# Optimization experiments

Hardware: AMD Instinct MI355X
Metric: run time of the kernel (lower is better)

The kernel has to match this reference:

```python
import jax, jax.numpy as jnp
import numpy as np

EMBED_SIZE = 768
HEAD_SIZE = 64
B, T = 4, 2048


def setup_inputs() -> dict:
    key = jax.random.key(0)
    kx, kk, kq, kv = jax.random.split(key, 4)
    x = jax.random.normal(kx, (B, T, EMBED_SIZE), dtype=jnp.float32)
    # torch Linear(E, H, bias=False): weight [H, E]; stored here as [E, H] for x @ W
    s = 1.0 / np.sqrt(EMBED_SIZE)
    Wk = jax.random.uniform(kk, (EMBED_SIZE, HEAD_SIZE), jnp.float32, -s, s)
    Wq = jax.random.uniform(kq, (EMBED_SIZE, HEAD_SIZE), jnp.float32, -s, s)
    Wv = jax.random.uniform(kv, (EMBED_SIZE, HEAD_SIZE), jnp.float32, -s, s)
    return {"x": x, "Wk": Wk, "Wq": Wq, "Wv": Wv}


def reference(x, Wk, Wq, Wv):
    Bx, Tx, E = x.shape
    k = x @ Wk  # [B, T, H]
    q = x @ Wq
    v = x @ Wv
    w = jnp.einsum("bth,bsh->bts", q, k)  # [B, T, T]
    causal = jnp.tril(jnp.ones((Tx, Tx), dtype=bool))
    # Faithful to source: mask to -inf FIRST, then scale by sqrt(embed_size)
    w = jnp.where(causal, w, -jnp.inf)
    w = w / jnp.sqrt(jnp.asarray(E, dtype=x.dtype))
    w = jax.nn.softmax(w, axis=-1)
    # dropout: eval mode / identity for the correctness baseline
    return jnp.einsum("bts,bsh->bth", w, v)
```

## Files before the change

kernel.cpp:

```cpp
#include <hip/hip_runtime.h>
#include <hip/hip_bf16.h>


typedef __attribute__((ext_vector_type(8))) short short8;
typedef __attribute__((ext_vector_type(4))) float f32x4;

#define SPLIT_KB 4
#define MAX_SP 8

__device__ __forceinline__ unsigned short f2bf(float f) {
    union { float f; unsigned u; } v; v.f = f;
    unsigned r = v.u + 0x7fffu + ((v.u >> 16) & 1u);
    return (unsigned short)(r >> 16);
}

__global__ __launch_bounds__(256) void proj_kernel(const float* __restrict__ x,
                                                   const float* __restrict__ Wk,
                                                   const float* __restrict__ Wq,
                                                   const float* __restrict__ Wv,
                                                   unsigned short* __restrict__ qws,
                                                   unsigned short* __restrict__ kws,
                                                   unsigned short* __restrict__ vT) {
    __shared__ unsigned short xs[32 * 72];
    __shared__ unsigned short wsm[64 * 72];
    const float CSCALE = 1.4426950408889634f / 27.712812921102035f;
    int tid = threadIdx.x;
    int lane = tid & 63, wave = tid >> 6;
    int quad = lane >> 4, l16 = lane & 15;
    int row0 = blockIdx.x * 32;
    int my = blockIdx.y;
    const float* W = (my == 0) ? Wq : (my == 1) ? Wk : Wv;

    int xrow = tid >> 3, xcb = (tid & 7) * 8;
    int wn = tid & 63, wk0 = (tid >> 6) * 16;

    f32x4 acc[2];
    acc[0] = (f32x4)(0.f); acc[1] = (f32x4)(0.f);

    for (int kc = 0; kc < 12; ++kc) {
        __syncthreads();
        {
            const float* src = x + (size_t)(row0 + xrow) * 768 + kc * 64 + xcb;
            float4 f0 = *(const float4*)(src);
            float4 f1 = *(const float4*)(src + 4);
            short8 pk;
            pk[0] = (short)f2bf(f0.x); pk[1] = (short)f2bf(f0.y);
            pk[2] = (short)f2bf(f0.z); pk[3] = (short)f2bf(f0.w);
            pk[4] = (short)f2bf(f1.x); pk[5] = (short)f2bf(f1.y);
            pk[6] = (short)f2bf(f1.z); pk[7] = (short)f2bf(f1.w);
            *(short8*)&xs[xrow * 72 + xcb] = pk;
        }
        {
            float wv[16];
            for (int i = 0; i < 16; ++i)
                wv[i] = W[(size_t)(kc * 64 + wk0 + i) * 64 + wn];
            if (my == 0)
                for (int i = 0; i < 16; ++i) wv[i] *= CSCALE;
            short8 p0, p1;
            for (int i = 0; i < 8; ++i) { p0[i] = (short)f2bf(wv[i]); p1[i] = (short)f2bf(wv[8 + i]); }
            *(short8*)&wsm[wn * 72 + wk0] = p0;
            *(short8*)&wsm[wn * 72 + wk0 + 8] = p1;
        }
        __syncthreads();
        for (int kh = 0; kh < 2; ++kh) {
            int kk = kh * 32 + quad * 8;
            short8 bfr = *(const short8*)&wsm[(wave * 16 + l16) * 72 + kk];
            for (int mt = 0; mt < 2; ++mt) {
                short8 a = *(const short8*)&xs[(mt * 16 + l16) * 72 + kk];
                acc[mt] = __builtin_amdgcn_mfma_f32_16x16x32_bf16(a, bfr, acc[mt], 0, 0, 0);
            }
        }
    }
    __syncthreads();
    int n = wave * 16 + l16;
    if (my != 2) {
        unsigned short* dst = (my == 0) ? qws : kws;
        for (int mt = 0; mt < 2; ++mt)
            for (int j = 0; j < 4; ++j) {
                int rloc = mt * 16 + quad * 4 + j;
                dst[(size_t)(row0 + rloc) * 64 + n] = f2bf(acc[mt][j]);
            }
    } else {
        for (int mt = 0; mt < 2; ++mt)
            for (int j = 0; j < 4; ++j) {
                int rloc = mt * 16 + quad * 4 + j;
                wsm[n * 40 + rloc] = f2bf(acc[mt][j]);
            }
        __syncthreads();
        int bidx = row0 >> 11, t0 = row0 & 2047;
        int c = tid >> 2, rb = (tid & 3) * 8;
        *(short8*)&vT[((size_t)(bidx * 64 + c)) * 2048 + t0 + rb] =
            *(const short8*)&wsm[c * 40 + rb];
    }
}

__global__ __launch_bounds__(128) void attn_split(const unsigned short* __restrict__ qws,
                                                  const unsigned short* __restrict__ kws,
                                                  const unsigned short* __restrict__ vT,
                                                  float* __restrict__ po,
                                                  float* __restrict__ pm,
                                                  float* __restrict__ pl,
                                                  float* __restrict__ out) {
    int bx = blockIdx.x, b = blockIdx.y, sp = blockIdx.z;
    int kbmax = (bx >> 1) + 1;
    int nsp = (kbmax + SPLIT_KB - 1) / SPLIT_KB;
    if (sp >= nsp) return;
    int kb_lo = sp * SPLIT_KB;
    int kb_hi = min(kb_lo + SPLIT_KB, kbmax);

    __shared__ unsigned short qs[32 * 72];
    __shared__ unsigned short ks[64 * 72];
    __shared__ unsigned short vs[64 * 72];
    __shared__ unsigned short ps[2][16 * 72];
    int tid = threadIdx.x;
    int lane = tid & 63, wave = tid >> 6;
    int quad = lane >> 4, l16 = lane & 15;
    int q0 = bx * 32;
    size_t qbase = ((size_t)b * 2048 + q0) * 64;
    for (int i = 0; i < 2; ++i) {
        int e = tid + 128 * i;
        int r = e >> 3, hb = (e & 7) * 8;
        *(short8*)&qs[r * 72 + hb] = *(const short8*)&qws[qbase + r * 64 + hb];
    }
    __syncthreads();
    short8 aq[2];
    for (int kh = 0; kh < 2; ++kh)
        aq[kh] = *(const short8*)&qs[(wave * 16 + l16) * 72 + kh * 32 + quad * 8];

    f32x4 o_acc[4];
    for (int nt = 0; nt < 4; ++nt) o_acc[nt] = (f32x4)(0.f);
    float m_run[4], l_run[4];
    int row_g[4];
    for (int j = 0; j < 4; ++j) {
        m_run[j] = -1e30f; l_run[j] = 0.f;
        row_g[j] = q0 + wave * 16 + quad * 4 + j;
    }

    for (int kb = kb_lo; kb < kb_hi; ++kb) {
        __syncthreads();
        size_t kvbase = ((size_t)b * 2048 + kb * 64) * 64;
        for (int i = 0; i < 4; ++i) {
            int e = tid + 128 * i;
            int r = e >> 3, hb = (e & 7) * 8;
            *(short8*)&ks[r * 72 + hb] = *(const short8*)&kws[kvbase + r * 64 + hb];
        }
        for (int i = 0; i < 4; ++i) {
            int e = tid + 128 * i;
            int h = e >> 3, kyb = (e & 7) * 8;
            *(short8*)&vs[h * 72 + kyb] =
                *(const short8*)&vT[((size_t)b * 64 + h) * 2048 + kb * 64 + kyb];
        }
        __syncthreads();
        f32x4 s[4];
        for (int nt = 0; nt < 4; ++nt) s[nt] = (f32x4)(0.f);
        for (int kh = 0; kh < 2; ++kh)
            for (int nt = 0; nt < 4; ++nt) {
                short8 bk = *(const short8*)&ks[(nt * 16 + l16) * 72 + kh * 32 + quad * 8];
                s[nt] = __builtin_amdgcn_mfma_f32_16x16x32_bf16(aq[kh], bk, s[nt], 0, 0, 0);
            }
        if (kb == kbmax - 1) {
            for (int nt = 0; nt < 4; ++nt) {
                int key = kb * 64 + nt * 16 + l16;
                for (int j = 0; j < 4; ++j)
                    if (key > row_g[j]) s[nt][j] = -1e30f;
            }
        }
        float mx[4], al[4], rs[4];
        for (int j = 0; j < 4; ++j)
            mx[j] = fmaxf(fmaxf(s[0][j], s[1][j]), fmaxf(s[2][j], s[3][j]));
        for (int off = 1; off < 16; off <<= 1)
            for (int j = 0; j < 4; ++j)
                mx[j] = fmaxf(mx[j], __shfl_xor(mx[j], off, 16));
        for (int j = 0; j < 4; ++j) {
            float mn = fmaxf(m_run[j], mx[j]);
            al[j] = exp2f(m_run[j] - mn);
            m_run[j] = mn;
            rs[j] = 0.f;
        }
        for (int nt = 0; nt < 4; ++nt)
            for (int j = 0; j < 4; ++j) {
                float p = exp2f(s[nt][j] - m_run[j]);
                rs[j] += p;
                ps[wave][(quad * 4 + j) * 72 + nt * 16 + l16] = f2bf(p);
            }
        for (int off = 1; off < 16; off <<= 1)
            for (int j = 0; j < 4; ++j)
                rs[j] += __shfl_xor(rs[j], off, 16);
        for (int j = 0; j < 4; ++j) l_run[j] = l_run[j] * al[j] + rs[j];
        for (int nt = 0; nt < 4; ++nt)
            for (int j = 0; j < 4; ++j) o_acc[nt][j] *= al[j];
        for (int kh = 0; kh < 2; ++kh) {
            short8 ap = *(const short8*)&ps[wave][l16 * 72 + kh * 32 + quad * 8];
            for (int nt = 0; nt < 4; ++nt) {
                short8 bv = *(const short8*)&vs[(nt * 16 + l16) * 72 + kh * 32 + quad * 8];
                o_acc[nt] = __builtin_amdgcn_mfma_f32_16x16x32_bf16(ap, bv, o_acc[nt], 0, 0, 0);
            }
        }
    }
    if (nsp == 1) {
        for (int nt = 0; nt < 4; ++nt)
            for (int j = 0; j < 4; ++j)
                out[((size_t)b * 2048 + row_g[j]) * 64 + nt * 16 + l16] =
                    o_acc[nt][j] / l_run[j];
        return;
    }
    int sbase = ((b * 64 + bx) * MAX_SP + sp) * 32;
    for (int nt = 0; nt < 4; ++nt)
        for (int j = 0; j < 4; ++j) {
            int r = wave * 16 + quad * 4 + j;
            po[(size_t)(sbase + r) * 64 + nt * 16 + l16] = o_acc[nt][j];
        }
    if (l16 == 0) {
        for (int j = 0; j < 4; ++j) {
            int r = wave * 16 + quad * 4 + j;
            pm[sbase + r] = m_run[j];
            pl[sbase + r] = l_run[j];
        }
    }
}

__global__ __launch_bounds__(256) void reduce_kernel(const float* __restrict__ po,
                                                     const float* __restrict__ pm,
                                                     const float* __restrict__ pl,
                                                     float* __restrict__ out) {
    int tid = threadIdx.x;
    int lane = tid & 63, wave = tid >> 6;
    int g = blockIdx.x * 4 + wave;
    int b = g >> 11, t = g & 2047;
    int bx = t >> 5, r = t & 31;
    int kbmax = (bx >> 1) + 1;
    int nsp = (kbmax + SPLIT_KB - 1) / SPLIT_KB;
    if (nsp == 1) return;
    int base = ((b * 64 + bx) * MAX_SP) * 32 + r;
    float mstar = -1e30f;
    for (int sp = 0; sp < nsp; ++sp)
        mstar = fmaxf(mstar, pm[base + sp * 32]);
    float acc = 0.f, lsum = 0.f;
    for (int sp = 0; sp < nsp; ++sp) {
        float w = exp2f(pm[base + sp * 32] - mstar);
        acc += w * po[(size_t)(base + sp * 32) * 64 + lane];
        lsum += w * pl[base + sp * 32];
    }
    out[(size_t)g * 64 + lane] = acc / lsum;
}

extern "C" void kernel_launch(void* const* d_in, const int* in_sizes, int n_in,
                              void* d_out, int out_size, void* d_ws, size_t ws_size,
                              hipStream_t stream) {
    const float* x  = (const float*)d_in[0];
    const float* Wk = (const float*)d_in[1];
    const float* Wq = (const float*)d_in[2];
    const float* Wv = (const float*)d_in[3];
    float* out = (float*)d_out;
    char* w = (char*)d_ws;
    unsigned short* qws = (unsigned short*)w;
    unsigned short* kws = (unsigned short*)(w + 1048576);
    unsigned short* vT  = (unsigned short*)(w + 2097152);
    float* po = (float*)(w + 3145728);
    float* pm = (float*)(w + 19922944);
    float* pl = (float*)(w + 20185088);
    proj_kernel<<<dim3(256, 3), 256, 0, stream>>>(x, Wk, Wq, Wv, qws, kws, vT);
    attn_split<<<dim3(64, 4, MAX_SP), 128, 0, stream>>>(qws, kws, vT, po, pm, pl, out);
    reduce_kernel<<<2048, 256, 0, stream>>>(po, pm, pl, out);
}
```

Baseline: 109.8 us.

## Use single-wave attention blocks loading K/V fragments directly from global memory

The attention kernel changes from 128-thread blocks covering 32 query rows to 64-thread single-wave blocks covering 16 rows, with twice as many blocks. Q, K and V MFMA operands are read straight from global memory into registers, so the shared-memory staging and the block barriers go away. Only a small per-wave P buffer stays in LDS. The price is that K/V reuse across waves is lost, so each wave fetches its own K/V tiles (L2 traffic roughly doubles), and the global loads are strided short8 reads.

```diff
diff --git a/kernel.cpp b/kernel.cpp
--- a/kernel.cpp
+++ b/kernel.cpp
@@ -94,38 +94,28 @@
     }
 }
 
-__global__ __launch_bounds__(128) void attn_split(const unsigned short* __restrict__ qws,
-                                                  const unsigned short* __restrict__ kws,
-                                                  const unsigned short* __restrict__ vT,
-                                                  float* __restrict__ po,
-                                                  float* __restrict__ pm,
-                                                  float* __restrict__ pl,
-                                                  float* __restrict__ out) {
+__global__ __launch_bounds__(64) void attn_split(const unsigned short* __restrict__ qws,
+                                                 const unsigned short* __restrict__ kws,
+                                                 const unsigned short* __restrict__ vT,
+                                                 float* __restrict__ po,
+                                                 float* __restrict__ pm,
+                                                 float* __restrict__ pl,
+                                                 float* __restrict__ out) {
     int bx = blockIdx.x, b = blockIdx.y, sp = blockIdx.z;
-    int kbmax = (bx >> 1) + 1;
+    int kbmax = (bx >> 2) + 1;
     int nsp = (kbmax + SPLIT_KB - 1) / SPLIT_KB;
     if (sp >= nsp) return;
     int kb_lo = sp * SPLIT_KB;
     int kb_hi = min(kb_lo + SPLIT_KB, kbmax);
 
-    __shared__ unsigned short qs[32 * 72];
-    __shared__ unsigned short ks[64 * 72];
-    __shared__ unsigned short vs[64 * 72];
-    __shared__ unsigned short ps[2][16 * 72];
-    int tid = threadIdx.x;
-    int lane = tid & 63, wave = tid >> 6;
+    __shared__ unsigned short ps[16 * 72];
+    int lane = threadIdx.x & 63;
     int quad = lane >> 4, l16 = lane & 15;
-    int q0 = bx * 32;
-    size_t qbase = ((size_t)b * 2048 + q0) * 64;
-    for (int i = 0; i < 2; ++i) {
-        int e = tid + 128 * i;
-        int r = e >> 3, hb = (e & 7) * 8;
-        *(short8*)&qs[r * 72 + hb] = *(const short8*)&qws[qbase + r * 64 + hb];
-    }
-    __syncthreads();
-    short8 aq[2];
-    for (int kh = 0; kh < 2; ++kh)
-        aq[kh] = *(const short8*)&qs[(wave * 16 + l16) * 72 + kh * 32 + quad * 8];
+    int q0 = bx * 16;
+
+    const unsigned short* qp = qws + ((size_t)b * 2048 + q0 + l16) * 64 + quad * 8;
+    short8 aq0 = *(const short8*)(qp);
+    short8 aq1 = *(const short8*)(qp + 32);
 
     f32x4 o_acc[4];
     for (int nt = 0; nt < 4; ++nt) o_acc[nt] = (f32x4)(0.f);
@@ -133,31 +123,20 @@
     int row_g[4];
     for (int j = 0; j < 4; ++j) {
         m_run[j] = -1e30f; l_run[j] = 0.f;
-        row_g[j] = q0 + wave * 16 + quad * 4 + j;
+        row_g[j] = q0 + quad * 4 + j;
     }
 
     for (int kb = kb_lo; kb < kb_hi; ++kb) {
-        __syncthreads();
-        size_t kvbase = ((size_t)b * 2048 + kb * 64) * 64;
-        for (int i = 0; i < 4; ++i) {
-            int e = tid + 128 * i;
-            int r = e >> 3, hb = (e & 7) * 8;
-            *(short8*)&ks[r * 72 + hb] = *(const short8*)&kws[kvbase + r * 64 + hb];
-        }
-        for (int i = 0; i < 4; ++i) {
-            int e = tid + 128 * i;
-            int h = e >> 3, kyb = (e & 7) * 8;
-            *(short8*)&vs[h * 72 + kyb] =
-                *(const short8*)&vT[((size_t)b * 64 + h) * 2048 + kb * 64 + kyb];
-        }
-        __syncthreads();
+        const unsigned short* kp =
+            kws + ((size_t)b * 2048 + kb * 64 + l16) * 64 + quad * 8;
         f32x4 s[4];
         for (int nt = 0; nt < 4; ++nt) s[nt] = (f32x4)(0.f);
-        for (int kh = 0; kh < 2; ++kh)
-            for (int nt = 0; nt < 4; ++nt) {
-                short8 bk = *(const short8*)&ks[(nt * 16 + l16) * 72 + kh * 32 + quad * 8];
-                s[nt] = __builtin_amdgcn_mfma_f32_16x16x32_bf16(aq[kh], bk, s[nt], 0, 0, 0);
-            }
+        for (int nt = 0; nt < 4; ++nt) {
+            short8 bk0 = *(const short8*)(kp + (size_t)nt * 16 * 64);
+            short8 bk1 = *(const short8*)(kp + (size_t)nt * 16 * 64 + 32);
+            s[nt] = __builtin_amdgcn_mfma_f32_16x16x32_bf16(aq0, bk0, s[nt], 0, 0, 0);
+            s[nt] = __builtin_amdgcn_mfma_f32_16x16x32_bf16(aq1, bk1, s[nt], 0, 0, 0);
+        }
         if (kb == kbmax - 1) {
             for (int nt = 0; nt < 4; ++nt) {
                 int key = kb * 64 + nt * 16 + l16;
@@ -181,7 +160,7 @@
             for (int j = 0; j < 4; ++j) {
                 float p = exp2f(s[nt][j] - m_run[j]);
                 rs[j] += p;
-                ps[wave][(quad * 4 + j) * 72 + nt * 16 + l16] = f2bf(p);
+                ps[(quad * 4 + j) * 72 + nt * 16 + l16] = f2bf(p);
             }
         for (int off = 1; off < 16; off <<= 1)
             for (int j = 0; j < 4; ++j)
@@ -189,10 +168,12 @@
         for (int j = 0; j < 4; ++j) l_run[j] = l_run[j] * al[j] + rs[j];
         for (int nt = 0; nt < 4; ++nt)
             for (int j = 0; j < 4; ++j) o_acc[nt][j] *= al[j];
+        const unsigned short* vp =
+            vT + ((size_t)b * 64 + l16) * 2048 + kb * 64 + quad * 8;
         for (int kh = 0; kh < 2; ++kh) {
-            short8 ap = *(const short8*)&ps[wave][l16 * 72 + kh * 32 + quad * 8];
+            short8 ap = *(const short8*)&ps[l16 * 72 + kh * 32 + quad * 8];
             for (int nt = 0; nt < 4; ++nt) {
-                short8 bv = *(const short8*)&vs[(nt * 16 + l16) * 72 + kh * 32 + quad * 8];
+                short8 bv = *(const short8*)(vp + (size_t)nt * 16 * 2048 + kh * 32);
                 o_acc[nt] = __builtin_amdgcn_mfma_f32_16x16x32_bf16(ap, bv, o_acc[nt], 0, 0, 0);
             }
         }
@@ -204,15 +185,15 @@
                     o_acc[nt][j] / l_run[j];
         return;
     }
-    int sbase = ((b * 64 + bx) * MAX_SP + sp) * 32;
+    int sbase = ((b * 128 + bx) * MAX_SP + sp) * 16;
     for (int nt = 0; nt < 4; ++nt)
         for (int j = 0; j < 4; ++j) {
-            int r = wave * 16 + quad * 4 + j;
+            int r = quad * 4 + j;
             po[(size_t)(sbase + r) * 64 + nt * 16 + l16] = o_acc[nt][j];
         }
     if (l16 == 0) {
         for (int j = 0; j < 4; ++j) {
-            int r = wave * 16 + quad * 4 + j;
+            int r = quad * 4 + j;
             pm[sbase + r] = m_run[j];
             pl[sbase + r] = l_run[j];
         }
@@ -227,19 +208,19 @@
     int lane = tid & 63, wave = tid >> 6;
     int g = blockIdx.x * 4 + wave;
     int b = g >> 11, t = g & 2047;
-    int bx = t >> 5, r = t & 31;
-    int kbmax = (bx >> 1) + 1;
+    int bx = t >> 4, r = t & 15;
+    int kbmax = (bx >> 2) + 1;
     int nsp = (kbmax + SPLIT_KB - 1) / SPLIT_KB;
     if (nsp == 1) return;
-    int base = ((b * 64 + bx) * MAX_SP) * 32 + r;
+    int base = ((b * 128 + bx) * MAX_SP) * 16 + r;
     float mstar = -1e30f;
     for (int sp = 0; sp < nsp; ++sp)
-        mstar = fmaxf(mstar, pm[base + sp * 32]);
+        mstar = fmaxf(mstar, pm[base + sp * 16]);
     float acc = 0.f, lsum = 0.f;
     for (int sp = 0; sp < nsp; ++sp) {
-        float w = exp2f(pm[base + sp * 32] - mstar);
-        acc += w * po[(size_t)(base + sp * 32) * 64 + lane];
-        lsum += w * pl[base + sp * 32];
+        float w = exp2f(pm[base + sp * 16] - mstar);
+        acc += w * po[(size_t)(base + sp * 16) * 64 + lane];
+        lsum += w * pl[base + sp * 16];
     }
     out[(size_t)g * 64 + lane] = acc / lsum;
 }
@@ -260,6 +241,6 @@
     float* pm = (float*)(w + 19922944);
     float* pl = (float*)(w + 20185088);
     proj_kernel<<<dim3(256, 3), 256, 0, stream>>>(x, Wk, Wq, Wv, qws, kws, vT);
-    attn_split<<<dim3(64, 4, MAX_SP), 128, 0, stream>>>(qws, kws, vT, po, pm, pl, out);
+    attn_split<<<dim3(128, 4, MAX_SP), 64, 0, stream>>>(qws, kws, vT, po, pm, pl, out);
     reduce_kernel<<<2048, 256, 0, stream>>>(po, pm, pl, out);
 }
```

Result: slower. 115.7 us (+5.3%).
